# Kernel tuning notes

Measured on AMD Instinct MI355X. Metric: run time of the kernel, lower is better.

The kernel has to match this reference:

```python
import jax, jax.numpy as jnp
import numpy as np

B, C_LEN, Q_LEN, D = 8, 2048, 512, 1024


def setup_inputs() -> dict:
    key = jax.random.key(0)
    ks = jax.random.split(key, 10)
    scale = 1.0 / np.sqrt(D)
    return {
        "c": jax.random.normal(ks[0], (B, C_LEN, D), dtype=jnp.float32),
        "q": jax.random.normal(ks[1], (B, Q_LEN, D), dtype=jnp.float32),
        "w_cq": jax.random.normal(ks[2], (D,), dtype=jnp.float32) * scale,
        "b_cq": jax.random.normal(ks[3], (), dtype=jnp.float32) * scale,
        "w_c": jax.random.normal(ks[4], (D,), dtype=jnp.float32) * scale,
        "b_c": jax.random.normal(ks[5], (), dtype=jnp.float32) * scale,
        "w_q": jax.random.normal(ks[6], (D,), dtype=jnp.float32) * scale,
        "b_q": jax.random.normal(ks[7], (), dtype=jnp.float32) * scale,
        "W_l": jax.random.normal(ks[8], (D, 4 * D), dtype=jnp.float32) * (1.0 / np.sqrt(4 * D)),
        "b_l": jax.random.normal(ks[9], (D,), dtype=jnp.float32) * (1.0 / np.sqrt(4 * D)),
    }


def reference(c, q, w_cq, b_cq, w_c, b_c, w_q, b_q, W_l, b_l):
    # trilinear term: the original loops over q positions computing
    # att_weight_cq(c * q_i); since that Linear is rank-1, this is one einsum.
    cq = jnp.einsum('bcd,bqd,d->bcq', c, q, w_cq) + b_cq        # [B, C, Q]
    s = (c @ w_c + b_c)[:, :, None] + (q @ w_q + b_q)[:, None, :] + cq
    a = jax.nn.softmax(s, axis=2)                               # c2q attention
    c2q_att = jnp.einsum('bcq,bqd->bcd', a, q)                  # [B, C, D]
    b_att = jax.nn.softmax(jnp.max(s, axis=2), axis=1)          # [B, C]
    q2c_att = jnp.einsum('bc,bcd->bd', b_att, c)[:, None, :]    # [B, 1, D]
    x = jnp.concatenate([c, c2q_att, c * c2q_att, c * q2c_att], axis=-1)
    z = x @ W_l.T + b_l                                         # [B, C, D]
    return z
```

## Files before the change

kernel.cpp:

```cpp
#include <hip/hip_runtime.h>

typedef unsigned short u16;
typedef __attribute__((ext_vector_type(4))) float floatx4;
typedef __attribute__((ext_vector_type(4))) unsigned short u16x4;
typedef __attribute__((ext_vector_type(8))) short short8;
typedef __attribute__((ext_vector_type(8))) __bf16 bf16x8;

#define B_SZ 8
#define C_LEN 2048
#define Q_LEN 512
#define D_DIM 1024
#define K4 (4 * D_DIM)

static __device__ __forceinline__ u16 f2bf(float f) {
    union { float f; unsigned int u; } v; v.f = f;
    unsigned int r = v.u + 0x7FFFu + ((v.u >> 16) & 1u);
    return (u16)(r >> 16);
}
static __device__ __forceinline__ float bf2f(u16 h) {
    union { unsigned int u; float f; } v; v.u = ((unsigned int)h) << 16;
    return v.f;
}

static __device__ __forceinline__ void async16(const void* g, void* l) {
    __builtin_amdgcn_global_load_lds(
        (const __attribute__((address_space(1))) unsigned int*)g,
        (__attribute__((address_space(3))) unsigned int*)(unsigned int)(unsigned long long)l,
        16, 0, 0);
}

__global__ __launch_bounds__(256) void prep_kernel(
    const float* __restrict__ c, const float* __restrict__ q,
    const float* __restrict__ w_cq, const float* __restrict__ w_c, const float* __restrict__ w_q,
    u16* __restrict__ cbf, u16* __restrict__ qwbf, u16* __restrict__ qT,
    float* __restrict__ rowterm, float* __restrict__ colterm, float* __restrict__ q2c) {
    int blk = blockIdx.x;
    int tid = threadIdx.x;
    if (blk < 4096) {
        int row = blk * 4 + (tid >> 6);
        int lane = tid & 63;
        const float* src = c + (size_t)row * D_DIM;
        u16* dst = cbf + (size_t)row * D_DIM;
        float s = 0.f;
        #pragma unroll
        for (int j = 0; j < 4; ++j) {
            int idx = j * 256 + lane * 4;
            floatx4 a = *(const floatx4*)(src + idx);
            floatx4 w = *(const floatx4*)(w_c + idx);
            s += a[0]*w[0] + a[1]*w[1] + a[2]*w[2] + a[3]*w[3];
            u16x4 o;
            #pragma unroll
            for (int e = 0; e < 4; ++e) o[e] = f2bf(a[e]);
            *(u16x4*)(dst + idx) = o;
        }
        for (int off = 32; off; off >>= 1) s += __shfl_down(s, off);
        if (lane == 0) rowterm[row] = s;
    } else if (blk < 5120) {
        int row = (blk - 4096) * 4 + (tid >> 6);
        int lane = tid & 63;
        const float* src = q + (size_t)row * D_DIM;
        u16* dst = qwbf + (size_t)row * D_DIM;
        float s = 0.f;
        #pragma unroll
        for (int j = 0; j < 4; ++j) {
            int idx = j * 256 + lane * 4;
            floatx4 a  = *(const floatx4*)(src + idx);
            floatx4 wc = *(const floatx4*)(w_cq + idx);
            floatx4 wq = *(const floatx4*)(w_q + idx);
            s += a[0]*wq[0] + a[1]*wq[1] + a[2]*wq[2] + a[3]*wq[3];
            u16x4 o;
            #pragma unroll
            for (int e = 0; e < 4; ++e) o[e] = f2bf(a[e] * wc[e]);
            *(u16x4*)(dst + idx) = o;
        }
        for (int off = 32; off; off >>= 1) s += __shfl_down(s, off);
        if (lane == 0) colterm[row] = s;
    } else if (blk < 9216) {
        __shared__ float tile[32][33];
        int t = blk - 5120;
        int q0 = (t & 15) * 32;
        int d0 = ((t >> 4) & 31) * 32;
        int b = t >> 9;
        int tx = tid & 31, ty = tid >> 5;
        const float* qb = q + (size_t)b * Q_LEN * D_DIM;
        #pragma unroll
        for (int j = 0; j < 4; ++j) {
            int row = ty + j * 8;
            tile[row][tx] = qb[(size_t)(q0 + row) * D_DIM + d0 + tx];
        }
        __syncthreads();
        u16* qTb = qT + (size_t)b * D_DIM * Q_LEN;
        #pragma unroll
        for (int j = 0; j < 4; ++j) {
            int row = ty + j * 8;
            qTb[(size_t)(d0 + row) * Q_LEN + q0 + tx] = f2bf(tile[tx][row]);
        }
    } else {
        int i = (blk - 9216) * 256 + tid;
        q2c[i] = 0.0f;
    }
}

__global__ __launch_bounds__(256) void wmerge_all(const float* __restrict__ W, const float* __restrict__ q2c,
                                                  u16* __restrict__ Wm, u16* __restrict__ Wbf) {
    int n = blockIdx.x;
    int k = threadIdx.x * 4;
    const float* wr = W + (size_t)n * K4;
    floatx4 w1 = *(const floatx4*)(wr + k);
    floatx4 w4 = *(const floatx4*)(wr + 3072 + k);
    #pragma unroll
    for (int p = 0; p < 2; ++p) {
        int kk = p * 1024 + k;
        floatx4 v = *(const floatx4*)(wr + 1024 + kk);
        u16x4 o;
        #pragma unroll
        for (int e = 0; e < 4; ++e) o[e] = f2bf(v[e]);
        *(u16x4*)(Wbf + (size_t)n * 2048 + kk) = o;
    }
    #pragma unroll
    for (int b = 0; b < 8; ++b) {
        floatx4 g = *(const floatx4*)(q2c + (size_t)b * D_DIM + k);
        u16x4 o;
        #pragma unroll
        for (int e = 0; e < 4; ++e) o[e] = f2bf(w1[e] + w4[e] * g[e]);
        *(u16x4*)(Wm + (size_t)b * 1048576 + (size_t)n * 1024 + k) = o;
    }
}

template<int MODE>
__global__ __launch_bounds__(256) void gemm_async(
    const u16* __restrict__ A0, const u16* __restrict__ A1, const u16* __restrict__ A2,
    const u16* __restrict__ B0, const u16* __restrict__ B1,
    float* __restrict__ of, u16* __restrict__ ob, const float* __restrict__ bias) {
    constexpr int NSEC = (MODE == 2) ? 3 : 1;
    constexpr int KSEC = (MODE == 1) ? 512 : 1024;
    constexpr int LDO  = (MODE == 0) ? 512 : 1024;
    constexpr int NTILES = (MODE == 0) ? 4 : 8;
    __shared__ u16 As[128 * 64];
    __shared__ u16 Bs[128 * 64];
    const int tid  = threadIdx.x;
    const int lane = tid & 63;
    const int wave = tid >> 6;
    const int lin  = blockIdx.x;
    const int b    = lin & 7;
    const int rem  = lin >> 3;
    const int n0   = (rem % NTILES) * 128;
    const int m0   = (rem / NTILES) * 128;

    const u16* Aarr[NSEC];
    const u16* Barr[NSEC];
    int lda_[NSEC], ldb_[NSEC];
    if constexpr (MODE == 0) {
        Aarr[0] = A0 + (size_t)b * C_LEN * D_DIM; lda_[0] = 1024;
        Barr[0] = B0 + (size_t)b * Q_LEN * D_DIM; ldb_[0] = 1024;
    } else if constexpr (MODE == 1) {
        Aarr[0] = A0 + (size_t)b * C_LEN * Q_LEN; lda_[0] = 512;
        Barr[0] = B0 + (size_t)b * D_DIM * Q_LEN; ldb_[0] = 512;
    } else {
        Aarr[0] = A0 + (size_t)b * C_LEN * D_DIM;  lda_[0] = 1024;
        Barr[0] = B0 + (size_t)b * D_DIM * D_DIM;  ldb_[0] = 1024;
        Aarr[1] = A1 + (size_t)b * C_LEN * 2048;        lda_[1] = 2048;
        Barr[1] = B1;                                   ldb_[1] = 2048;
        Aarr[2] = A1 + (size_t)b * C_LEN * 2048 + 1024; lda_[2] = 2048;
        Barr[2] = B1 + 1024;                            ldb_[2] = 2048;
    }

    const int srow = lane >> 3;
    const int ssc  = ((lane & 7) ^ srow) * 8;

    floatx4 acc[4][4];
    #pragma unroll
    for (int i = 0; i < 4; ++i)
        #pragma unroll
        for (int j = 0; j < 4; ++j)
            acc[i][j] = (floatx4)(0.0f);

    const int wrow = (wave >> 1) * 64;
    const int wcol = (wave & 1) * 64;
    const int quad = lane >> 4;
    const int lrow = lane & 15;
    const int sw7  = lane & 7;

    #pragma unroll
    for (int sec = 0; sec < NSEC; ++sec) {
        const u16* __restrict__ Ab = Aarr[sec];
        const u16* __restrict__ Bb = Barr[sec];
        const int LA = lda_[sec];
        const int LB = ldb_[sec];
        for (int k0 = 0; k0 < KSEC; k0 += 64) {
            #pragma unroll
            for (int cc = 0; cc < 4; ++cc) {
                int ch = wave * 4 + cc;
                int rr = ch * 8 + srow;
                async16(Ab + (size_t)(m0 + rr) * LA + k0 + ssc, &As[ch * 512]);
            }
            #pragma unroll
            for (int cc = 0; cc < 4; ++cc) {
                int ch = wave * 4 + cc;
                int rr = ch * 8 + srow;
                async16(Bb + (size_t)(n0 + rr) * LB + k0 + ssc, &Bs[ch * 512]);
            }
            __syncthreads();
            #pragma unroll
            for (int h = 0; h < 2; ++h) {
                const int pc = ((h * 4 + quad) ^ sw7) * 8;
                bf16x8 af[4], bfr[4];
                #pragma unroll
                for (int i = 0; i < 4; ++i)
                    af[i] = __builtin_bit_cast(bf16x8, *(const short8*)&As[(wrow + i*16 + lrow) * 64 + pc]);
                #pragma unroll
                for (int j = 0; j < 4; ++j)
                    bfr[j] = __builtin_bit_cast(bf16x8, *(const short8*)&Bs[(wcol + j*16 + lrow) * 64 + pc]);
                #pragma unroll
                for (int i = 0; i < 4; ++i)
                    #pragma unroll
                    for (int j = 0; j < 4; ++j)
                        acc[i][j] = __builtin_amdgcn_mfma_f32_16x16x32_bf16(af[i], bfr[j], acc[i][j], 0, 0, 0);
            }
            __syncthreads();
        }
    }

    float* ofb = nullptr; u16* ccb = nullptr; const u16* cbr = nullptr;
    if (MODE == 0)      ofb = of + (size_t)b * C_LEN * Q_LEN;
    else if (MODE == 1) { ccb = ob + (size_t)b * C_LEN * 2048; cbr = A1 + (size_t)b * C_LEN * D_DIM; }
    else                ofb = of + (size_t)b * C_LEN * D_DIM;
    #pragma unroll
    for (int i = 0; i < 4; ++i) {
        #pragma unroll
        for (int j = 0; j < 4; ++j) {
            #pragma unroll
            for (int e = 0; e < 4; ++e) {
                int gm = m0 + wrow + i * 16 + quad * 4 + e;
                int gn = n0 + wcol + j * 16 + lrow;
                float v = acc[i][j][e];
                if (MODE == 0)      ofb[(size_t)gm * LDO + gn] = v;
                else if (MODE == 1) {
                    u16 p = f2bf(v);
                    float cv = bf2f(cbr[(size_t)gm * 1024 + gn]);
                    ccb[(size_t)gm * 2048 + gn]        = p;
                    ccb[(size_t)gm * 2048 + 1024 + gn] = f2bf(cv * bf2f(p));
                }
                else                ofb[(size_t)gm * LDO + gn] = v + bias[gn];
            }
        }
    }
}

#define BAR8() __builtin_amdgcn_s_barrier()
#define VMW(N) do { asm volatile("s_waitcnt vmcnt(" #N ")" ::: "memory"); } while (0)

#define LDA4(DST, MQ, KH, CUR) do { \
    const u16* un_ = lds_ + (CUR) * 32768; \
    _Pragma("unroll") \
    for (int i_ = 0; i_ < 4; ++i_) \
      (DST)[i_] = __builtin_bit_cast(bf16x8, \
          *(const short8*)(un_ + (wm * 128 + (MQ) * 64 + i_ * 16 + lrow) * 64 + pca[KH])); \
  } while (0)

#define LDB4(DST, KH, CUR) do { \
    const u16* un_ = lds_ + (CUR) * 32768 + 16384; \
    _Pragma("unroll") \
    for (int i_ = 0; i_ < 4; ++i_) \
      (DST)[i_] = __builtin_bit_cast(bf16x8, \
          *(const short8*)(un_ + (wn * 64 + i_ * 16 + lrow) * 64 + pca[KH])); \
  } while (0)

#define MFMA16(MQ4, A_, B_) do { \
    __builtin_amdgcn_s_setprio(1); \
    _Pragma("unroll") \
    for (int i_ = 0; i_ < 4; ++i_) { \
      _Pragma("unroll") \
      for (int j_ = 0; j_ < 4; ++j_) \
        acc[(MQ4) + i_][j_] = __builtin_amdgcn_mfma_f32_16x16x32_bf16( \
            (A_)[i_], (B_)[j_], acc[(MQ4) + i_][j_], 0, 0, 0); \
    } \
    __builtin_amdgcn_s_setprio(0); \
  } while (0)

__global__ __launch_bounds__(512, 2) void gemm2_8ph(
    const u16* __restrict__ cbf, const u16* __restrict__ CC,
    const u16* __restrict__ Wm, const u16* __restrict__ Wbf,
    float* __restrict__ of, const float* __restrict__ bias) {
    __shared__ __align__(16) u16 lds_[65536];
    const int tid  = threadIdx.x;
    const int lane = tid & 63;
    const int wave = tid >> 6;
    const int lin  = blockIdx.x;
    const int b    = lin & 7;
    const int rem  = lin >> 3;
    const int n0   = (rem & 3) * 256;
    const int m0   = (rem >> 2) * 256;
    const int wm   = wave >> 2;
    const int wn   = wave & 3;
    const int quad = lane >> 4;
    const int lrow = lane & 15;
    const int lr7  = lane & 7;
    const int pca[2] = { ((0 + quad) ^ lr7) * 8, ((4 + quad) ^ lr7) * 8 };

    const u16* Acb  = cbf + (size_t)b * (C_LEN * D_DIM);
    const u16* Acc0 = CC  + (size_t)b * (C_LEN * 2048);
    const u16* Acc1 = Acc0 + 1024;
    const u16* Bwm  = Wm  + (size_t)b * (D_DIM * D_DIM);

    auto STAGE = [&](int tt, int ab) {
        const int sec = tt >> 4;
        const int kl  = (tt & 15) * 64;
        const u16* base;
        int r0;
        if (ab == 0) { base = (sec == 0) ? Acb : (sec == 1) ? Acc0 : Acc1; r0 = m0; }
        else         { base = (sec == 0) ? Bwm : (sec == 1) ? Wbf  : Wbf + 1024; r0 = n0; }
        const int ld = (sec == 0) ? 1024 : 2048;
        u16* unit = lds_ + (tt & 1) * 32768 + ab * 16384;
        #pragma unroll
        for (int l = 0; l < 4; ++l) {
            const int li  = l * 512 + tid;
            const int row = li >> 3;
            const int sc  = (li & 7) ^ (row & 7);
            async16(base + (size_t)(r0 + row) * ld + kl + sc * 8,
                    unit + (size_t)(l * 512 + (tid & ~63)) * 8);
        }
    };

    floatx4 acc[8][4];
    #pragma unroll
    for (int i = 0; i < 8; ++i)
        #pragma unroll
        for (int j = 0; j < 4; ++j) acc[i][j] = (floatx4)(0.0f);

    STAGE(0, 0); STAGE(0, 1); STAGE(1, 1);
    VMW(4);
    BAR8();

    bf16x8 af[4], bf[4];
    for (int tt = 0; tt < 48; ++tt) {
        const int cur = tt & 1;
        if (tt + 1 < 48) STAGE(tt + 1, 0);
        LDA4(af, 0, 0, cur);
        LDB4(bf, 0, cur);
        BAR8();
        MFMA16(0, af, bf);
        BAR8();
        LDA4(af, 1, 0, cur);
        BAR8();
        MFMA16(4, af, bf);
        BAR8();
        LDA4(af, 0, 1, cur);
        LDB4(bf, 1, cur);
        BAR8();
        MFMA16(0, af, bf);
        BAR8();
        if (tt + 2 < 48) STAGE(tt + 2, 1);
        LDA4(af, 1, 1, cur);
        BAR8();
        MFMA16(4, af, bf);
        if (tt < 46) { VMW(4); } else { VMW(0); }
        BAR8();
    }

    float bs[4];
    #pragma unroll
    for (int j = 0; j < 4; ++j) bs[j] = bias[n0 + wn * 64 + j * 16 + lrow];
    float* ofb = of + (size_t)b * (C_LEN * D_DIM);
    #pragma unroll
    for (int i = 0; i < 8; ++i) {
        #pragma unroll
        for (int j = 0; j < 4; ++j) {
            #pragma unroll
            for (int e = 0; e < 4; ++e) {
                const int gm = m0 + wm * 128 + i * 16 + quad * 4 + e;
                const int gn = n0 + wn * 64 + j * 16 + lrow;
                ofb[(size_t)gm * D_DIM + gn] = acc[i][j][e] + bs[j];
            }
        }
    }
}

__global__ void softmax_kernel(const float* __restrict__ S, const float* __restrict__ colterm,
                               u16* __restrict__ P, float* __restrict__ mbuf) {
    int row = blockIdx.x * 4 + (threadIdx.x >> 6);
    int lane = threadIdx.x & 63;
    int b = row >> 11;
    const float* sp = S + (size_t)row * Q_LEN;
    const float* cp = colterm + (size_t)b * Q_LEN;
    float v[8];
    float m = -1e30f;
    #pragma unroll
    for (int j = 0; j < 8; ++j) {
        int idx = j * 64 + lane;
        v[j] = sp[idx] + cp[idx];
        m = fmaxf(m, v[j]);
    }
    for (int off = 32; off; off >>= 1) m = fmaxf(m, __shfl_xor(m, off));
    float s = 0.f;
    #pragma unroll
    for (int j = 0; j < 8; ++j) { v[j] = __expf(v[j] - m); s += v[j]; }
    for (int off = 32; off; off >>= 1) s += __shfl_xor(s, off);
    float inv = 1.0f / s;
    u16* pp = P + (size_t)row * Q_LEN;
    #pragma unroll
    for (int j = 0; j < 8; ++j) pp[j * 64 + lane] = f2bf(v[j] * inv);
    if (lane == 0) mbuf[row] = m;
}

__global__ __launch_bounds__(256) void batt_kernel(const float* __restrict__ mbuf,
                                                   const float* __restrict__ rowterm,
                                                   float* __restrict__ batt) {
    __shared__ float red[8];
    int b = blockIdx.x;
    int tid = threadIdx.x;
    const float* mb = mbuf + (size_t)b * C_LEN;
    const float* rt = rowterm + (size_t)b * C_LEN;
    float v[8];
    float m = -1e30f;
    #pragma unroll
    for (int j = 0; j < 8; ++j) { int idx = j * 256 + tid; v[j] = mb[idx] + rt[idx]; m = fmaxf(m, v[j]); }
    for (int off = 32; off; off >>= 1) m = fmaxf(m, __shfl_xor(m, off));
    int wave = tid >> 6, lane = tid & 63;
    if (lane == 0) red[wave] = m;
    __syncthreads();
    m = fmaxf(fmaxf(red[0], red[1]), fmaxf(red[2], red[3]));
    float s = 0.f;
    #pragma unroll
    for (int j = 0; j < 8; ++j) { v[j] = __expf(v[j] - m); s += v[j]; }
    for (int off = 32; off; off >>= 1) s += __shfl_xor(s, off);
    if (lane == 0) red[4 + wave] = s;
    __syncthreads();
    s = red[4] + red[5] + red[6] + red[7];
    float inv = 1.0f / s;
    float* bb = batt + (size_t)b * C_LEN;
    #pragma unroll
    for (int j = 0; j < 8; ++j) bb[j * 256 + tid] = v[j] * inv;
}

__global__ __launch_bounds__(256) void q2c_kernel(const float* __restrict__ batt,
                                                  const u16* __restrict__ cbf,
                                                  float* __restrict__ q2c) {
    int d  = blockIdx.x * 256 + threadIdx.x;
    int b  = blockIdx.y;
    int c0 = blockIdx.z * 256;
    const u16* cb = cbf + ((size_t)b * C_LEN + c0) * D_DIM + d;
    const float* bb = batt + (size_t)b * C_LEN + c0;
    float s = 0.f;
    #pragma unroll 4
    for (int i = 0; i < 256; ++i) s += bb[i] * bf2f(cb[(size_t)i * D_DIM]);
    atomicAdd(&q2c[(size_t)b * D_DIM + d], s);
}

extern "C" void kernel_launch(void* const* d_in, const int* in_sizes, int n_in,
                              void* d_out, int out_size, void* d_ws, size_t ws_size,
                              hipStream_t stream) {
    const float* c   = (const float*)d_in[0];
    const float* q   = (const float*)d_in[1];
    const float* wcq = (const float*)d_in[2];
    const float* w_c = (const float*)d_in[4];
    const float* w_q = (const float*)d_in[6];
    const float* W_l = (const float*)d_in[8];
    const float* b_l = (const float*)d_in[9];
    float* out = (float*)d_out;

    char* ws = (char*)d_ws;
    u16*   cbf     = (u16*)ws;
    float* S       = (float*)(ws + 33554432);
    u16*   CC      = (u16*)(ws + 33554432);
    u16*   qwbf    = (u16*)(ws + 67108864);
    u16*   P       = (u16*)(ws + 100663296);
    u16*   Wm      = (u16*)(ws + 100663296);
    u16*   qT      = (u16*)(ws + 117440512);
    u16*   Wbf     = (u16*)(ws + 117440512);
    float* rowterm = (float*)(ws + 125829120);
    float* colterm = (float*)(ws + 125894656);
    float* mbuf    = (float*)(ws + 125911040);
    float* batt    = (float*)(ws + 125976576);
    float* q2c     = (float*)(ws + 126042112);

    prep_kernel<<<dim3(9248), dim3(256), 0, stream>>>(c, q, wcq, w_c, w_q,
                                                      cbf, qwbf, qT, rowterm, colterm, q2c);
    gemm_async<0><<<dim3(512), dim3(256), 0, stream>>>(cbf, nullptr, nullptr, qwbf, nullptr, S, nullptr, nullptr);
    softmax_kernel<<<dim3(4096), dim3(256), 0, stream>>>(S, colterm, P, mbuf);
    batt_kernel<<<dim3(8), dim3(256), 0, stream>>>(mbuf, rowterm, batt);
    q2c_kernel<<<dim3(4, 8, 8), dim3(256), 0, stream>>>(batt, cbf, q2c);
    gemm_async<1><<<dim3(1024), dim3(256), 0, stream>>>(P, cbf, nullptr, qT, nullptr, nullptr, CC, nullptr);
    wmerge_all<<<dim3(1024), dim3(256), 0, stream>>>(W_l, q2c, Wm, Wbf);
    gemm2_8ph<<<dim3(256), dim3(512), 0, stream>>>(cbf, CC, Wm, Wbf, out, b_l);
}
```

Before: 346.9 us.

## Restructure final GEMM into four quadrant phases with half-tile staging

The main output GEMM now splits each wave's work into four quadrant accumulators (row/column halves of the 256x256 tile) rather than two M-halves. Global-to-LDS staging is broken into half-tiles and spread across the four phases, which interleaves loads with MFMA work more finely. Explicit lgkmcnt waits are added so LDS reads complete before each MFMA batch. This aims to improve overlap of memory traffic with compute and to change the LDS fragment reuse pattern. The trade-off is more barriers and more careful ordering, which risks read-after-write hazards on the double-buffered LDS halves.

```diff
diff --git a/kernel.cpp b/kernel.cpp
--- a/kernel.cpp
+++ b/kernel.cpp
@@ -249,36 +249,43 @@
 
 #define BAR8() __builtin_amdgcn_s_barrier()
 #define VMW(N) do { asm volatile("s_waitcnt vmcnt(" #N ")" ::: "memory"); } while (0)
-
-#define LDA4(DST, MQ, KH, CUR) do { \
-    const u16* un_ = lds_ + (CUR) * 32768; \
+#define LGK0() do { asm volatile("s_waitcnt lgkmcnt(0)" ::: "memory"); } while (0)
+#define LGK8() do { asm volatile("s_waitcnt lgkmcnt(8)" ::: "memory"); } while (0)
+
+#define RD_A(QM, CUR) do { \
+    const u16* ua_ = lds_ + (CUR) * 32768; \
     _Pragma("unroll") \
-    for (int i_ = 0; i_ < 4; ++i_) \
-      (DST)[i_] = __builtin_bit_cast(bf16x8, \
-          *(const short8*)(un_ + (wm * 128 + (MQ) * 64 + i_ * 16 + lrow) * 64 + pca[KH])); \
+    for (int mi_ = 0; mi_ < 4; ++mi_) \
+      _Pragma("unroll") \
+      for (int kh_ = 0; kh_ < 2; ++kh_) \
+        afr[mi_*2+kh_] = __builtin_bit_cast(bf16x8, \
+            *(const short8*)(ua_ + ((QM)*128 + wr*64 + mi_*16 + lrow) * 64 + pca[kh_])); \
   } while (0)
 
-#define LDB4(DST, KH, CUR) do { \
-    const u16* un_ = lds_ + (CUR) * 32768 + 16384; \
+#define RD_B(QN, CUR) do { \
+    const u16* ub_ = lds_ + (CUR) * 32768 + 16384; \
     _Pragma("unroll") \
-    for (int i_ = 0; i_ < 4; ++i_) \
-      (DST)[i_] = __builtin_bit_cast(bf16x8, \
-          *(const short8*)(un_ + (wn * 64 + i_ * 16 + lrow) * 64 + pca[KH])); \
+    for (int ni_ = 0; ni_ < 2; ++ni_) \
+      _Pragma("unroll") \
+      for (int kh_ = 0; kh_ < 2; ++kh_) \
+        bfr[ni_*2+kh_] = __builtin_bit_cast(bf16x8, \
+            *(const short8*)(ub_ + ((QN)*128 + wc*32 + ni_*16 + lrow) * 64 + pca[kh_])); \
   } while (0)
 
-#define MFMA16(MQ4, A_, B_) do { \
+#define MM16(ACC) do { \
     __builtin_amdgcn_s_setprio(1); \
     _Pragma("unroll") \
-    for (int i_ = 0; i_ < 4; ++i_) { \
+    for (int kh_ = 0; kh_ < 2; ++kh_) \
       _Pragma("unroll") \
-      for (int j_ = 0; j_ < 4; ++j_) \
-        acc[(MQ4) + i_][j_] = __builtin_amdgcn_mfma_f32_16x16x32_bf16( \
-            (A_)[i_], (B_)[j_], acc[(MQ4) + i_][j_], 0, 0, 0); \
-    } \
+      for (int mi_ = 0; mi_ < 4; ++mi_) \
+        _Pragma("unroll") \
+        for (int ni_ = 0; ni_ < 2; ++ni_) \
+          ACC[mi_*2+ni_] = __builtin_amdgcn_mfma_f32_16x16x32_bf16( \
+              afr[mi_*2+kh_], bfr[ni_*2+kh_], ACC[mi_*2+ni_], 0, 0, 0); \
     __builtin_amdgcn_s_setprio(0); \
   } while (0)
 
-__global__ __launch_bounds__(512, 2) void gemm2_8ph(
+__global__ __launch_bounds__(512, 2) void gemm2_8q(
     const u16* __restrict__ cbf, const u16* __restrict__ CC,
     const u16* __restrict__ Wm, const u16* __restrict__ Wbf,
     float* __restrict__ of, const float* __restrict__ bias) {
@@ -291,8 +298,8 @@
     const int rem  = lin >> 3;
     const int n0   = (rem & 3) * 256;
     const int m0   = (rem >> 2) * 256;
-    const int wm   = wave >> 2;
-    const int wn   = wave & 3;
+    const int wr   = wave >> 2;
+    const int wc   = wave & 3;
     const int quad = lane >> 4;
     const int lrow = lane & 15;
     const int lr7  = lane & 7;
@@ -303,17 +310,18 @@
     const u16* Acc1 = Acc0 + 1024;
     const u16* Bwm  = Wm  + (size_t)b * (D_DIM * D_DIM);
 
-    auto STAGE = [&](int tt, int ab) {
+    auto STAGE = [&](int tt, int ab, int hf) {
         const int sec = tt >> 4;
         const int kl  = (tt & 15) * 64;
         const u16* base;
         int r0;
         if (ab == 0) { base = (sec == 0) ? Acb : (sec == 1) ? Acc0 : Acc1; r0 = m0; }
         else         { base = (sec == 0) ? Bwm : (sec == 1) ? Wbf  : Wbf + 1024; r0 = n0; }
+        r0 += hf * 128;
         const int ld = (sec == 0) ? 1024 : 2048;
-        u16* unit = lds_ + (tt & 1) * 32768 + ab * 16384;
-        #pragma unroll
-        for (int l = 0; l < 4; ++l) {
+        u16* unit = lds_ + (tt & 1) * 32768 + ab * 16384 + hf * 8192;
+        #pragma unroll
+        for (int l = 0; l < 2; ++l) {
             const int li  = l * 512 + tid;
             const int row = li >> 3;
             const int sc  = (li & 7) ^ (row & 7);
@@ -322,55 +330,71 @@
         }
     };
 
-    floatx4 acc[8][4];
-    #pragma unroll
-    for (int i = 0; i < 8; ++i)
-        #pragma unroll
-        for (int j = 0; j < 4; ++j) acc[i][j] = (floatx4)(0.0f);
-
-    STAGE(0, 0); STAGE(0, 1); STAGE(1, 1);
+    floatx4 acc0[8], acc1[8], acc2[8], acc3[8];
+    #pragma unroll
+    for (int i = 0; i < 8; ++i) {
+        acc0[i] = (floatx4)(0.0f); acc1[i] = (floatx4)(0.0f);
+        acc2[i] = (floatx4)(0.0f); acc3[i] = (floatx4)(0.0f);
+    }
+
+    STAGE(0, 0, 0); STAGE(0, 1, 0); STAGE(0, 0, 1); STAGE(0, 1, 1);
+    STAGE(1, 1, 0); STAGE(1, 0, 1);
     VMW(4);
     BAR8();
 
-    bf16x8 af[4], bf[4];
+    bf16x8 afr[8], bfr[4];
     for (int tt = 0; tt < 48; ++tt) {
         const int cur = tt & 1;
-        if (tt + 1 < 48) STAGE(tt + 1, 0);
-        LDA4(af, 0, 0, cur);
-        LDB4(bf, 0, cur);
-        BAR8();
-        MFMA16(0, af, bf);
-        BAR8();
-        LDA4(af, 1, 0, cur);
-        BAR8();
-        MFMA16(4, af, bf);
-        BAR8();
-        LDA4(af, 0, 1, cur);
-        LDB4(bf, 1, cur);
-        BAR8();
-        MFMA16(0, af, bf);
-        BAR8();
-        if (tt + 2 < 48) STAGE(tt + 2, 1);
-        LDA4(af, 1, 1, cur);
-        BAR8();
-        MFMA16(4, af, bf);
+        RD_A(0, cur);
+        RD_B(0, cur);
+        if (tt + 1 < 48) STAGE(tt + 1, 1, 1);
+        LGK8();
+        BAR8();
+        LGK0();
+        MM16(acc0);
+        BAR8();
+        RD_A(1, cur);
+        if (tt + 1 < 48) STAGE(tt + 1, 0, 0);
+        BAR8();
+        LGK0();
+        MM16(acc1);
+        BAR8();
+        RD_B(1, cur);
+        if (tt + 2 < 48) STAGE(tt + 2, 1, 0);
+        BAR8();
+        LGK0();
+        MM16(acc2);
+        BAR8();
+        RD_A(0, cur);
+        if (tt + 2 < 48) STAGE(tt + 2, 0, 1);
+        BAR8();
+        LGK0();
+        MM16(acc3);
         if (tt < 46) { VMW(4); } else { VMW(0); }
         BAR8();
     }
 
-    float bs[4];
-    #pragma unroll
-    for (int j = 0; j < 4; ++j) bs[j] = bias[n0 + wn * 64 + j * 16 + lrow];
+    float bs[2][2];
+    #pragma unroll
+    for (int qn = 0; qn < 2; ++qn)
+        #pragma unroll
+        for (int ni = 0; ni < 2; ++ni)
+            bs[qn][ni] = bias[n0 + qn * 128 + wc * 32 + ni * 16 + lrow];
     float* ofb = of + (size_t)b * (C_LEN * D_DIM);
     #pragma unroll
-    for (int i = 0; i < 8; ++i) {
-        #pragma unroll
-        for (int j = 0; j < 4; ++j) {
+    for (int mi = 0; mi < 4; ++mi) {
+        #pragma unroll
+        for (int ni = 0; ni < 2; ++ni) {
             #pragma unroll
             for (int e = 0; e < 4; ++e) {
-                const int gm = m0 + wm * 128 + i * 16 + quad * 4 + e;
-                const int gn = n0 + wn * 64 + j * 16 + lrow;
-                ofb[(size_t)gm * D_DIM + gn] = acc[i][j][e] + bs[j];
+                const int rA = m0 + wr * 64 + mi * 16 + quad * 4 + e;
+                const int rB = rA + 128;
+                const int cA = n0 + wc * 32 + ni * 16 + lrow;
+                const int cB = cA + 128;
+                ofb[(size_t)rA * D_DIM + cA] = acc0[mi*2+ni][e] + bs[0][ni];
+                ofb[(size_t)rB * D_DIM + cA] = acc1[mi*2+ni][e] + bs[0][ni];
+                ofb[(size_t)rB * D_DIM + cB] = acc2[mi*2+ni][e] + bs[1][ni];
+                ofb[(size_t)rA * D_DIM + cB] = acc3[mi*2+ni][e] + bs[1][ni];
             }
         }
     }
@@ -482,5 +506,5 @@
     q2c_kernel<<<dim3(4, 8, 8), dim3(256), 0, stream>>>(batt, cbf, q2c);
     gemm_async<1><<<dim3(1024), dim3(256), 0, stream>>>(P, cbf, nullptr, qT, nullptr, nullptr, CC, nullptr);
     wmerge_all<<<dim3(1024), dim3(256), 0, stream>>>(W_l, q2c, Wm, Wbf);
-    gemm2_8ph<<<dim3(256), dim3(512), 0, stream>>>(cbf, CC, Wm, Wbf, out, b_l);
-}
+    gemm2_8q<<<dim3(256), dim3(512), 0, stream>>>(cbf, CC, Wm, Wbf, out, b_l);
+}
```

Measured after the change: 351.5 us. About the same (+1.3%).
